# Kernel tuning notes

Hardware: AMD Instinct MI355X
Metric: run time of the kernel (lower is better)

The kernel has to match this reference:

```python
import jax, jax.numpy as jnp
import numpy as np


def setup_inputs() -> dict:
    key = jax.random.key(0)
    k1, k2, k3, k4, k5, k6 = jax.random.split(key, 6)
    B, C, H, W = 32, 512, 56, 56
    KD = 768
    x = jax.random.normal(k1, (B, C, H, W), dtype=jnp.float32)
    keyword = jax.random.normal(k2, (B, KD), dtype=jnp.float32)
    # Conv2d(2, 1, kernel_size=7): torch kaiming-uniform-ish init scale
    fan_in_conv = 2 * 7 * 7
    bnd_c = 1.0 / np.sqrt(fan_in_conv)
    conv_w = jax.random.uniform(k3, (1, 2, 7, 7), jnp.float32, -bnd_c, bnd_c)  # OIHW
    conv_b = jax.random.uniform(k4, (1,), jnp.float32, -bnd_c, bnd_c)
    # Linear(KD, 1)
    bnd_l = 1.0 / np.sqrt(KD)
    proj_w = jax.random.uniform(k5, (1, KD), jnp.float32, -bnd_l, bnd_l)
    proj_b = jax.random.uniform(k6, (1,), jnp.float32, -bnd_l, bnd_l)
    return {"x": x, "keyword": keyword, "conv_w": conv_w, "conv_b": conv_b,
            "proj_w": proj_w, "proj_b": proj_b}


def reference(x, keyword, conv_w, conv_b, proj_w, proj_b):
    # channel-wise max+mean pool -> [B, 2, H, W]
    x_compress = jnp.concatenate(
        [jnp.max(x, axis=1, keepdims=True), jnp.mean(x, axis=1, keepdims=True)],
        axis=1)
    # 7x7 conv, 2->1 channels, SAME padding (pad=3)
    attention = jax.lax.conv_general_dilated(
        x_compress, conv_w, window_strides=(1, 1), padding=[(3, 3), (3, 3)],
        dimension_numbers=("NCHW", "OIHW", "NCHW"))
    attention = attention + conv_b[None, :, None, None]  # [B,1,H,W]
    # keyword bias: Linear(KD->1), broadcast over H,W
    keyword_bias = keyword @ proj_w.T + proj_b  # [B,1]
    attention = attention + keyword_bias[:, :, None, None]
    scale = jax.nn.sigmoid(attention)
    return x * scale
```

## Files before the change

kernel.cpp:

```cpp
#include <hip/hip_runtime.h>
#include <math.h>

#define B 32
#define C 512
#define H 56
#define W 56
#define HW (H * W)
#define HW4 (HW / 4)
#define KD 768

typedef float floatx4 __attribute__((ext_vector_type(4)));

__global__ __launch_bounds__(512) void pool_kernel(
    const float* __restrict__ x, float* __restrict__ cmax, float* __restrict__ cmean) {
    const int tid = threadIdx.x;
    const int pos = tid & 31;
    const int cg  = tid >> 5;
    const int p   = blockIdx.x * 32 + pos;
    const int b   = p / HW4;
    const int hw4 = p - b * HW4;

    const floatx4* xb = (const floatx4*)x + (size_t)b * C * HW4 + hw4;

    floatx4 mx = { -INFINITY, -INFINITY, -INFINITY, -INFINITY };
    floatx4 sm = { 0.f, 0.f, 0.f, 0.f };
    const int c0 = cg * 32;
    #pragma unroll 4
    for (int c = c0; c < c0 + 32; ++c) {
        floatx4 v = xb[(size_t)c * HW4];
        mx.x = fmaxf(mx.x, v.x); mx.y = fmaxf(mx.y, v.y);
        mx.z = fmaxf(mx.z, v.z); mx.w = fmaxf(mx.w, v.w);
        sm += v;
    }

    __shared__ floatx4 smax[16][32];
    __shared__ floatx4 ssum[16][32];
    smax[cg][pos] = mx;
    ssum[cg][pos] = sm;
    __syncthreads();

    if (tid < 32) {
        mx = smax[0][tid];
        sm = ssum[0][tid];
        #pragma unroll
        for (int g = 1; g < 16; ++g) {
            floatx4 m2 = smax[g][tid];
            mx.x = fmaxf(mx.x, m2.x); mx.y = fmaxf(mx.y, m2.y);
            mx.z = fmaxf(mx.z, m2.z); mx.w = fmaxf(mx.w, m2.w);
            sm += ssum[g][tid];
        }
        const float inv = 1.0f / (float)C;
        floatx4 mn = sm * inv;
        const int pp = blockIdx.x * 32 + tid;
        ((floatx4*)cmax)[pp]  = mx;
        ((floatx4*)cmean)[pp] = mn;
    }
}

__global__ __launch_bounds__(256) void bias_kernel(
    const float* __restrict__ keyword, const float* __restrict__ proj_w,
    const float* __restrict__ proj_b, float* __restrict__ bias) {
    const int b   = blockIdx.x;
    const int tid = threadIdx.x;
    float s = 0.f;
    for (int k = tid; k < KD; k += 256)
        s += keyword[b * KD + k] * proj_w[k];
    #pragma unroll
    for (int off = 32; off > 0; off >>= 1)
        s += __shfl_down(s, off);
    __shared__ float warp_s[4];
    if ((tid & 63) == 0) warp_s[tid >> 6] = s;
    __syncthreads();
    if (tid == 0)
        bias[b] = warp_s[0] + warp_s[1] + warp_s[2] + warp_s[3] + proj_b[0];
}

__global__ __launch_bounds__(256) void conv_kernel(
    const float* __restrict__ cmax, const float* __restrict__ cmean,
    const float* __restrict__ conv_w, const float* __restrict__ conv_b,
    const float* __restrict__ bias, float* __restrict__ scale) {
    __shared__ float wsm[98];
    __shared__ float cb;
    const int tid = threadIdx.x;
    if (tid < 98) wsm[tid] = conv_w[tid];
    if (tid == 98) cb = conv_b[0];
    __syncthreads();

    const int o  = blockIdx.x * 256 + tid;
    const int b  = o / HW;
    const int hw = o - b * HW;
    const int h  = hw / W;
    const int w  = hw - h * W;

    float acc = cb + bias[b];
    const float* cmx = cmax  + b * HW;
    const float* cmn = cmean + b * HW;
    #pragma unroll
    for (int kh = 0; kh < 7; ++kh) {
        const int ih = h + kh - 3;
        if (ih < 0 || ih >= H) continue;
        #pragma unroll
        for (int kw = 0; kw < 7; ++kw) {
            const int iw = w + kw - 3;
            if (iw < 0 || iw >= W) continue;
            const int idx = ih * W + iw;
            acc = fmaf(cmx[idx], wsm[kh * 7 + kw],
                  fmaf(cmn[idx], wsm[49 + kh * 7 + kw], acc));
        }
    }
    scale[o] = 1.0f / (1.0f + __expf(-acc));
}

__global__ __launch_bounds__(256) void scale_kernel(
    const floatx4* __restrict__ x4, const floatx4* __restrict__ scale4,
    floatx4* __restrict__ out4) {
    const int base = blockIdx.x * 1024 + threadIdx.x;
    #pragma unroll
    for (int k = 0; k < 4; ++k) {
        const int v    = base + k * 256;
        const int rowv = v / HW4;
        const int hwv  = v - rowv * HW4;
        const int b    = rowv >> 9;
        floatx4 xv = __builtin_nontemporal_load(&x4[v]);
        floatx4 sv = scale4[b * HW4 + hwv];
        floatx4 o  = xv * sv;
        __builtin_nontemporal_store(o, &out4[v]);
    }
}

extern "C" void kernel_launch(void* const* d_in, const int* in_sizes, int n_in,
                              void* d_out, int out_size, void* d_ws, size_t ws_size,
                              hipStream_t stream) {
    const float* x       = (const float*)d_in[0];
    const float* keyword = (const float*)d_in[1];
    const float* conv_w  = (const float*)d_in[2];
    const float* conv_b  = (const float*)d_in[3];
    const float* proj_w  = (const float*)d_in[4];
    const float* proj_b  = (const float*)d_in[5];
    float* out = (float*)d_out;

    float* ws    = (float*)d_ws;
    float* cmax  = ws;
    float* cmean = ws + B * HW;
    float* scale = ws + 2 * B * HW;
    float* bias  = ws + 3 * B * HW;

    bias_kernel<<<B, 256, 0, stream>>>(keyword, proj_w, proj_b, bias);
    pool_kernel<<<(B * HW4) / 32, 512, 0, stream>>>(x, cmax, cmean);
    conv_kernel<<<(B * HW) / 256, 256, 0, stream>>>(cmax, cmean, conv_w, conv_b, bias, scale);
    scale_kernel<<<(B * C * HW4) / 1024, 256, 0, stream>>>(
        (const floatx4*)x, (const floatx4*)scale, (float4*)out ? (floatx4*)out : (floatx4*)out);
}
```

Baseline: 391.5 us.

## Fuse keyword bias, 7x7 conv and scaling into one banded kernel

Replaces separate bias, conv and scale kernels with one kernel where each block handles a 4-row band of one image across a 64-channel group. The block recomputes the keyword bias and the band's conv into shared memory, then multiplies x by the local scale. This removes two launches and the global scale-map round trip, at the cost of redundant conv and bias computation per channel group.

Result: faster. 383.2 us (-2.1%).

```diff
diff --git a/kernel.cpp b/kernel.cpp
--- a/kernel.cpp
+++ b/kernel.cpp
@@ -8,6 +8,13 @@
 #define HW (H * W)
 #define HW4 (HW / 4)
 #define KD 768
+
+#define BAND 4
+#define NBAND (H / BAND)
+#define CG 64
+#define NCG (C / CG)
+#define HROWS (BAND + 6)
+#define HCOLS (W + 6)
 
 typedef float floatx4 __attribute__((ext_vector_type(4)));
 
@@ -57,74 +64,76 @@
     }
 }
 
-__global__ __launch_bounds__(256) void bias_kernel(
+__global__ __launch_bounds__(256) void fused_kernel(
+    const float* __restrict__ cmax, const float* __restrict__ cmean,
+    const float* __restrict__ conv_w, const float* __restrict__ conv_b,
     const float* __restrict__ keyword, const float* __restrict__ proj_w,
-    const float* __restrict__ proj_b, float* __restrict__ bias) {
-    const int b   = blockIdx.x;
-    const int tid = threadIdx.x;
-    float s = 0.f;
-    for (int k = tid; k < KD; k += 256)
-        s += keyword[b * KD + k] * proj_w[k];
+    const float* __restrict__ proj_b,
+    const floatx4* __restrict__ x4, floatx4* __restrict__ out4) {
+    __shared__ float sm[2][HROWS][HCOLS];
+    __shared__ float s_w[98];
+    __shared__ __align__(16) float s_scale[BAND * W];
+    __shared__ float s_red[4];
+
+    const int tid  = threadIdx.x;
+    const int bid  = blockIdx.x;
+    const int cg   = bid & (NCG - 1);
+    const int rest = bid >> 3;
+    const int band = rest % NBAND;
+    const int b    = rest / NBAND;
+    const int row0 = band * BAND;
+
+    if (tid < 98) s_w[tid] = conv_w[tid];
+
+    float part = keyword[b * KD + tid]       * proj_w[tid]
+               + keyword[b * KD + tid + 256] * proj_w[tid + 256]
+               + keyword[b * KD + tid + 512] * proj_w[tid + 512];
     #pragma unroll
     for (int off = 32; off > 0; off >>= 1)
-        s += __shfl_down(s, off);
-    __shared__ float warp_s[4];
-    if ((tid & 63) == 0) warp_s[tid >> 6] = s;
-    __syncthreads();
-    if (tid == 0)
-        bias[b] = warp_s[0] + warp_s[1] + warp_s[2] + warp_s[3] + proj_b[0];
-}
+        part += __shfl_down(part, off);
+    if ((tid & 63) == 0) s_red[tid >> 6] = part;
 
-__global__ __launch_bounds__(256) void conv_kernel(
-    const float* __restrict__ cmax, const float* __restrict__ cmean,
-    const float* __restrict__ conv_w, const float* __restrict__ conv_b,
-    const float* __restrict__ bias, float* __restrict__ scale) {
-    __shared__ float wsm[98];
-    __shared__ float cb;
-    const int tid = threadIdx.x;
-    if (tid < 98) wsm[tid] = conv_w[tid];
-    if (tid == 98) cb = conv_b[0];
+    for (int idx = tid; idx < 2 * HROWS * HCOLS; idx += 256) {
+        const int m   = idx / (HROWS * HCOLS);
+        const int rem = idx - m * (HROWS * HCOLS);
+        const int r   = rem / HCOLS;
+        const int j   = rem - r * HCOLS;
+        const int ih  = row0 - 3 + r;
+        const int iw  = j - 3;
+        float v = 0.f;
+        if (ih >= 0 && ih < H && iw >= 0 && iw < W)
+            v = (m == 0 ? cmax : cmean)[b * HW + ih * W + iw];
+        sm[m][r][j] = v;
+    }
     __syncthreads();
 
-    const int o  = blockIdx.x * 256 + tid;
-    const int b  = o / HW;
-    const int hw = o - b * HW;
-    const int h  = hw / W;
-    const int w  = hw - h * W;
+    if (tid < BAND * W) {
+        const int dr  = tid / W;
+        const int col = tid - dr * W;
+        float acc = s_red[0] + s_red[1] + s_red[2] + s_red[3]
+                  + proj_b[0] + conv_b[0];
+        #pragma unroll
+        for (int kh = 0; kh < 7; ++kh) {
+            #pragma unroll
+            for (int kw = 0; kw < 7; ++kw) {
+                acc = fmaf(sm[0][dr + kh][col + kw], s_w[kh * 7 + kw],
+                      fmaf(sm[1][dr + kh][col + kw], s_w[49 + kh * 7 + kw], acc));
+            }
+        }
+        s_scale[tid] = 1.0f / (1.0f + __expf(-acc));
+    }
+    __syncthreads();
 
-    float acc = cb + bias[b];
-    const float* cmx = cmax  + b * HW;
-    const float* cmn = cmean + b * HW;
-    #pragma unroll
-    for (int kh = 0; kh < 7; ++kh) {
-        const int ih = h + kh - 3;
-        if (ih < 0 || ih >= H) continue;
-        #pragma unroll
-        for (int kw = 0; kw < 7; ++kw) {
-            const int iw = w + kw - 3;
-            if (iw < 0 || iw >= W) continue;
-            const int idx = ih * W + iw;
-            acc = fmaf(cmx[idx], wsm[kh * 7 + kw],
-                  fmaf(cmn[idx], wsm[49 + kh * 7 + kw], acc));
-        }
-    }
-    scale[o] = 1.0f / (1.0f + __expf(-acc));
-}
-
-__global__ __launch_bounds__(256) void scale_kernel(
-    const floatx4* __restrict__ x4, const floatx4* __restrict__ scale4,
-    floatx4* __restrict__ out4) {
-    const int base = blockIdx.x * 1024 + threadIdx.x;
-    #pragma unroll
-    for (int k = 0; k < 4; ++k) {
-        const int v    = base + k * 256;
-        const int rowv = v / HW4;
-        const int hwv  = v - rowv * HW4;
-        const int b    = rowv >> 9;
-        floatx4 xv = __builtin_nontemporal_load(&x4[v]);
-        floatx4 sv = scale4[b * HW4 + hwv];
-        floatx4 o  = xv * sv;
-        __builtin_nontemporal_store(o, &out4[v]);
+    const floatx4* s4 = (const floatx4*)s_scale;
+    const size_t base = (size_t)(b * C + cg * CG) * HW4 + band * (BAND * W / 4);
+    #pragma unroll 2
+    for (int i = tid; i < CG * (BAND * W / 4); i += 256) {
+        const int cl = i / 56;
+        const int f  = i - cl * 56;
+        const size_t g = base + (size_t)cl * HW4 + f;
+        floatx4 xv = __builtin_nontemporal_load(&x4[g]);
+        floatx4 ov = xv * s4[f];
+        __builtin_nontemporal_store(ov, &out4[g]);
     }
 }
 
@@ -142,12 +151,9 @@
     float* ws    = (float*)d_ws;
     float* cmax  = ws;
     float* cmean = ws + B * HW;
-    float* scale = ws + 2 * B * HW;
-    float* bias  = ws + 3 * B * HW;
 
-    bias_kernel<<<B, 256, 0, stream>>>(keyword, proj_w, proj_b, bias);
     pool_kernel<<<(B * HW4) / 32, 512, 0, stream>>>(x, cmax, cmean);
-    conv_kernel<<<(B * HW) / 256, 256, 0, stream>>>(cmax, cmean, conv_w, conv_b, bias, scale);
-    scale_kernel<<<(B * C * HW4) / 1024, 256, 0, stream>>>(
-        (const floatx4*)x, (const floatx4*)scale, (float4*)out ? (floatx4*)out : (floatx4*)out);
+    fused_kernel<<<B * NBAND * NCG, 256, 0, stream>>>(
+        cmax, cmean, conv_w, conv_b, keyword, proj_w, proj_b,
+        (const floatx4*)x, (floatx4*)out);
 }
```
